# Kernel tuning notes

Hardware: AMD Instinct MI355X
Metric: run time of the kernel (lower is better)

The kernel has to match this reference:

```python
import jax, jax.numpy as jnp
import numpy as np

B = 16384      # number of ragged groups (batch)
SEG = 50       # history length per group -> sum(size)
TGT = 10       # targets per group -> sum(target_size)
H = 64         # hidden_size
NU = 1_000_000 # num_users
NI = 1_000_000 # num_items
TOTAL = B * SEG
T = B * TGT


def setup_inputs() -> dict:
    key = jax.random.key(0)
    k1, k2, k3, k4, k5 = jax.random.split(key, 5)
    user = jax.random.randint(k1, (TOTAL,), 0, NU)
    item = jax.random.randint(k2, (TOTAL,), 0, NI)
    target_item = jax.random.randint(k3, (T,), 0, NI)
    size = jnp.full((B,), SEG, dtype=jnp.int32)
    target_size = jnp.full((B,), TGT, dtype=jnp.int32)
    # nn.init.normal_(w, 0.0, 1e-4)
    user_weight = jax.random.normal(k4, (NU, H), dtype=jnp.float32) * 1e-4
    item_weight = jax.random.normal(k5, (NI, H), dtype=jnp.float32) * 1e-4
    return {"user": user, "item": item, "target_item": target_item,
            "size": size, "target_size": target_size,
            "user_weight": user_weight, "item_weight": item_weight}


def _center_l2(x):
    # F.normalize(x - x.mean(-1, keepdims=True), dim=-1)
    x = x - x.mean(axis=-1, keepdims=True)
    n = jnp.sqrt(jnp.sum(x * x, axis=-1, keepdims=True))
    return x / jnp.maximum(n, 1e-12)


def reference(user, item, target_item, size, target_size, user_weight, item_weight):
    nb = size.shape[0]
    total = item.shape[0]
    t = target_item.shape[0]
    # last user index of each segment: cumsum(size) - 1
    last_idx = jnp.cumsum(size) - 1
    user_emb = user_weight[user[last_idx]]                      # [B, H]
    item_emb = item_weight[item]                                # [total, H]
    seg_ids = jnp.repeat(jnp.arange(nb), size, total_repeat_length=total)
    seg_sum = jax.ops.segment_sum(item_emb, seg_ids, num_segments=nb)  # [B, H]
    item_mean = seg_sum / (size.astype(seg_sum.dtype)[:, None] + 1e-6)
    emb = 0.5 * user_emb + 0.5 * item_mean                      # [B, H]
    emb = jnp.repeat(emb, target_size, axis=0, total_repeat_length=t)  # [T, H]
    tgt_emb = item_weight[target_item]                          # [T, H]
    emb = _center_l2(emb)
    tgt_emb = _center_l2(tgt_emb)
    simplex = jnp.sum(emb * tgt_emb, axis=-1)                   # [T]
    return simplex
```

## Files before the change

### kernel.cpp

```cpp
#include <hip/hip_runtime.h>

#define HDIM 64

__device__ __forceinline__ float sub16_sum(float v) {
  v += __shfl_xor(v, 1);
  v += __shfl_xor(v, 2);
  v += __shfl_xor(v, 4);
  v += __shfl_xor(v, 8);
  return v;
}

__global__ void scan_offsets(const int* __restrict__ size,
                             const int* __restrict__ tsize, int B,
                             int* __restrict__ seg_off,
                             int* __restrict__ tgt_off) {
  __shared__ int s1[256];
  __shared__ int s2[256];
  const int t = threadIdx.x;
  const int per = (B + 255) >> 8;
  const int base = t * per;
  int sum1 = 0, sum2 = 0;
  for (int i = 0; i < per; ++i) {
    const int j = base + i;
    if (j < B) { sum1 += size[j]; sum2 += tsize[j]; }
  }
  s1[t] = sum1; s2[t] = sum2;
  __syncthreads();
  for (int d = 1; d < 256; d <<= 1) {
    const int a1 = (t >= d) ? s1[t - d] : 0;
    const int a2 = (t >= d) ? s2[t - d] : 0;
    __syncthreads();
    s1[t] += a1; s2[t] += a2;
    __syncthreads();
  }
  int ex1 = (t > 0) ? s1[t - 1] : 0;
  int ex2 = (t > 0) ? s2[t - 1] : 0;
  for (int i = 0; i < per; ++i) {
    const int j = base + i;
    if (j < B) {
      seg_off[j] = ex1; tgt_off[j] = ex2;
      ex1 += size[j];   ex2 += tsize[j];
    }
  }
}

__global__ __launch_bounds__(256) void simplex_kernel(
    const int* __restrict__ user, const int* __restrict__ item,
    const int* __restrict__ target_item, const int* __restrict__ size,
    const int* __restrict__ tsize, const float* __restrict__ uw,
    const float* __restrict__ iw, const int* __restrict__ seg_off,
    const int* __restrict__ tgt_off, float* __restrict__ out, int B,
    int useg, int utgt) {
  const int g = (int)((blockIdx.x * blockDim.x + threadIdx.x) >> 6);
  if (g >= B) return;
  const int lane = threadIdx.x & 63;
  const int sub = lane >> 4;
  const int c4 = lane & 15;

  const int sz = size[g];
  const int tn = tsize[g];
  int off, toff;
  if (seg_off) { off = seg_off[g]; toff = tgt_off[g]; }
  else         { off = g * useg;   toff = g * utgt; }

  float4 acc = make_float4(0.f, 0.f, 0.f, 0.f);
  for (int base = 0; base < sz; base += 64) {
    const int nrem = sz - base;
    const int nchunk = nrem < 64 ? nrem : 64;
    const int idx = (lane < nrem) ? item[off + base + lane] : 0;
#pragma unroll
    for (int i = 0; i < 64; i += 4) {
      const int r = i + sub;
      const int row = __shfl(idx, r);
      if (r < nchunk) {
        const float4 v = *reinterpret_cast<const float4*>(
            iw + (size_t)row * HDIM + (c4 << 2));
        acc.x += v.x; acc.y += v.y; acc.z += v.z; acc.w += v.w;
      }
    }
  }
  acc.x += __shfl_xor(acc.x, 16); acc.y += __shfl_xor(acc.y, 16);
  acc.z += __shfl_xor(acc.z, 16); acc.w += __shfl_xor(acc.w, 16);
  acc.x += __shfl_xor(acc.x, 32); acc.y += __shfl_xor(acc.y, 32);
  acc.z += __shfl_xor(acc.z, 32); acc.w += __shfl_xor(acc.w, 32);

  const float inv_sz = 1.0f / ((float)sz + 1e-6f);

  const int u = user[off + sz - 1];
  const float4 ue = *reinterpret_cast<const float4*>(
      uw + (size_t)u * HDIM + (c4 << 2));

  float4 e;
  e.x = 0.5f * ue.x + 0.5f * (acc.x * inv_sz);
  e.y = 0.5f * ue.y + 0.5f * (acc.y * inv_sz);
  e.z = 0.5f * ue.z + 0.5f * (acc.z * inv_sz);
  e.w = 0.5f * ue.w + 0.5f * (acc.w * inv_sz);

  const float mu = sub16_sum(e.x + e.y + e.z + e.w) * (1.0f / 64.0f);
  e.x -= mu; e.y -= mu; e.z -= mu; e.w -= mu;
  const float ss = sub16_sum(e.x * e.x + e.y * e.y + e.z * e.z + e.w * e.w);
  const float einv = 1.0f / fmaxf(sqrtf(ss), 1e-12f);
  e.x *= einv; e.y *= einv; e.z *= einv; e.w *= einv;

  for (int tb = 0; tb < tn; tb += 64) {
    const int trem = tn - tb;
    const int tch = trem < 64 ? trem : 64;
    const int tidx = (lane < trem) ? target_item[toff + tb + lane] : 0;
    for (int j = 0; j < tch; j += 4) {
      const int r = j + sub;
      const bool valid = r < tch;
      const int row = __shfl(tidx, r);
      float4 tv = make_float4(0.f, 0.f, 0.f, 0.f);
      if (valid) {
        tv = *reinterpret_cast<const float4*>(
            iw + (size_t)row * HDIM + (c4 << 2));
      }
      const float tmu = sub16_sum(tv.x + tv.y + tv.z + tv.w) * (1.0f / 64.0f);
      tv.x -= tmu; tv.y -= tmu; tv.z -= tmu; tv.w -= tmu;
      float tss = tv.x * tv.x + tv.y * tv.y + tv.z * tv.z + tv.w * tv.w;
      float dt  = e.x * tv.x + e.y * tv.y + e.z * tv.z + e.w * tv.w;
#pragma unroll
      for (int m = 1; m <= 8; m <<= 1) {
        tss += __shfl_xor(tss, m);
        dt  += __shfl_xor(dt, m);
      }
      if (valid && c4 == 0) {
        out[toff + tb + r] = dt / fmaxf(sqrtf(tss), 1e-12f);
      }
    }
  }
}

extern "C" void kernel_launch(void* const* d_in, const int* in_sizes, int n_in,
                              void* d_out, int out_size, void* d_ws,
                              size_t ws_size, hipStream_t stream) {
  const int* user        = (const int*)d_in[0];
  const int* item        = (const int*)d_in[1];
  const int* target_item = (const int*)d_in[2];
  const int* size        = (const int*)d_in[3];
  const int* tsize       = (const int*)d_in[4];
  const float* uw        = (const float*)d_in[5];
  const float* iw        = (const float*)d_in[6];
  float* out             = (float*)d_out;

  const int TOTAL = in_sizes[0];
  const int T     = in_sizes[2];
  const int B     = in_sizes[3];
  const int useg  = TOTAL / B;
  const int utgt  = T / B;

  int* seg_off = nullptr;
  int* tgt_off = nullptr;
  if (ws_size >= (size_t)2 * (size_t)B * sizeof(int)) {
    seg_off = (int*)d_ws;
    tgt_off = seg_off + B;
    scan_offsets<<<1, 256, 0, stream>>>(size, tsize, B, seg_off, tgt_off);
  }

  const int block = 256;
  const long long threads = (long long)B * 64;
  const int grid = (int)((threads + block - 1) / block);
  simplex_kernel<<<grid, block, 0, stream>>>(user, item, target_item, size,
                                             tsize, uw, iw, seg_off, tgt_off,
                                             out, B, useg, utgt);
}
```

Measured before the change: 500.5 us.

## Parallelize offset scan and batch all gathers upfront in fast path

Replaces the single-block offset scan with a two-level multi-block scan (per-block scan plus a one-wave scan of block totals), removing a serial prologue kernel. Adds a fast path for segments of at most 64 items and 16 targets that issues all 16 history-row loads, 4 target-row loads and the user-row load before any arithmetic, so many gathers are in flight at once. Branches in the loops are replaced by clamped indices and zero-weight FMAs. This raises register pressure and adds one extra kernel launch, and out-of-range rows are fetched redundantly.

```diff
diff --git a/kernel.cpp b/kernel.cpp
--- a/kernel.cpp
+++ b/kernel.cpp
@@ -1,6 +1,54 @@
 #include <hip/hip_runtime.h>
 
 #define HDIM 64
+
+
+__global__ __launch_bounds__(256) void scan_blocks(
+    const int* __restrict__ size, const int* __restrict__ tsize, int B,
+    int* __restrict__ seg_loc, int* __restrict__ tgt_loc,
+    int* __restrict__ seg_tot, int* __restrict__ tgt_tot) {
+  __shared__ int s1[256];
+  __shared__ int s2[256];
+  const int t = threadIdx.x;
+  const int i = blockIdx.x * 256 + t;
+  const int a = (i < B) ? size[i] : 0;
+  const int b = (i < B) ? tsize[i] : 0;
+  s1[t] = a; s2[t] = b;
+  __syncthreads();
+#pragma unroll
+  for (int d = 1; d < 256; d <<= 1) {
+    const int v1 = (t >= d) ? s1[t - d] : 0;
+    const int v2 = (t >= d) ? s2[t - d] : 0;
+    __syncthreads();
+    s1[t] += v1; s2[t] += v2;
+    __syncthreads();
+  }
+  if (i < B) { seg_loc[i] = s1[t] - a; tgt_loc[i] = s2[t] - b; }
+  if (t == 255) { seg_tot[blockIdx.x] = s1[255]; tgt_tot[blockIdx.x] = s2[255]; }
+}
+
+__global__ void scan_totals(int nb, int* __restrict__ seg_tot,
+                            int* __restrict__ tgt_tot,
+                            int* __restrict__ seg_base,
+                            int* __restrict__ tgt_base) {
+  const int lane = threadIdx.x & 63;
+  int c1 = 0, c2 = 0;
+  for (int base = 0; base < nb; base += 64) {
+    const int i = base + lane;
+    const int a0 = (i < nb) ? seg_tot[i] : 0;
+    const int b0 = (i < nb) ? tgt_tot[i] : 0;
+    int a = a0, b = b0;
+#pragma unroll
+    for (int d = 1; d < 64; d <<= 1) {
+      const int xa = __shfl_up(a, d);
+      const int xb = __shfl_up(b, d);
+      if (lane >= d) { a += xa; b += xb; }
+    }
+    if (i < nb) { seg_base[i] = c1 + a - a0; tgt_base[i] = c2 + b - b0; }
+    c1 += __shfl(a, 63);
+    c2 += __shfl(b, 63);
+  }
+}
 
 __device__ __forceinline__ float sub16_sum(float v) {
   v += __shfl_xor(v, 1);
@@ -10,46 +58,13 @@
   return v;
 }
 
-__global__ void scan_offsets(const int* __restrict__ size,
-                             const int* __restrict__ tsize, int B,
-                             int* __restrict__ seg_off,
-                             int* __restrict__ tgt_off) {
-  __shared__ int s1[256];
-  __shared__ int s2[256];
-  const int t = threadIdx.x;
-  const int per = (B + 255) >> 8;
-  const int base = t * per;
-  int sum1 = 0, sum2 = 0;
-  for (int i = 0; i < per; ++i) {
-    const int j = base + i;
-    if (j < B) { sum1 += size[j]; sum2 += tsize[j]; }
-  }
-  s1[t] = sum1; s2[t] = sum2;
-  __syncthreads();
-  for (int d = 1; d < 256; d <<= 1) {
-    const int a1 = (t >= d) ? s1[t - d] : 0;
-    const int a2 = (t >= d) ? s2[t - d] : 0;
-    __syncthreads();
-    s1[t] += a1; s2[t] += a2;
-    __syncthreads();
-  }
-  int ex1 = (t > 0) ? s1[t - 1] : 0;
-  int ex2 = (t > 0) ? s2[t - 1] : 0;
-  for (int i = 0; i < per; ++i) {
-    const int j = base + i;
-    if (j < B) {
-      seg_off[j] = ex1; tgt_off[j] = ex2;
-      ex1 += size[j];   ex2 += tsize[j];
-    }
-  }
-}
-
 __global__ __launch_bounds__(256) void simplex_kernel(
     const int* __restrict__ user, const int* __restrict__ item,
     const int* __restrict__ target_item, const int* __restrict__ size,
     const int* __restrict__ tsize, const float* __restrict__ uw,
-    const float* __restrict__ iw, const int* __restrict__ seg_off,
-    const int* __restrict__ tgt_off, float* __restrict__ out, int B,
+    const float* __restrict__ iw, const int* __restrict__ seg_loc,
+    const int* __restrict__ tgt_loc, const int* __restrict__ seg_base,
+    const int* __restrict__ tgt_base, float* __restrict__ out, int B,
     int useg, int utgt) {
   const int g = (int)((blockIdx.x * blockDim.x + threadIdx.x) >> 6);
   if (g >= B) return;
@@ -60,10 +75,84 @@
   const int sz = size[g];
   const int tn = tsize[g];
   int off, toff;
-  if (seg_off) { off = seg_off[g]; toff = tgt_off[g]; }
-  else         { off = g * useg;   toff = g * utgt; }
+  if (seg_loc) {
+    off = seg_base[g >> 8] + seg_loc[g];
+    toff = tgt_base[g >> 8] + tgt_loc[g];
+  } else {
+    off = g * useg;
+    toff = g * utgt;
+  }
+
+  const int szc = (sz > 0) ? sz : 1;
+  const int tnc = (tn > 0) ? tn : 1;
 
   float4 acc = make_float4(0.f, 0.f, 0.f, 0.f);
+
+  if (sz <= 64 && tn <= 16) {
+    const int idx = item[off + ((lane < szc) ? lane : (szc - 1))];
+    const int tidx = target_item[toff + ((lane < tnc) ? lane : (tnc - 1))];
+    const int u = user[off + szc - 1];
+
+    float4 sv[16];
+#pragma unroll
+    for (int p = 0; p < 16; ++p) {
+      const int r = p * 4 + sub;
+      const int row = __shfl(idx, (r < szc) ? r : (szc - 1));
+      sv[p] = *reinterpret_cast<const float4*>(iw + ((size_t)row << 6) + (c4 << 2));
+    }
+    float4 tv[4];
+#pragma unroll
+    for (int p = 0; p < 4; ++p) {
+      const int r = p * 4 + sub;
+      const int row = __shfl(tidx, (r < tnc) ? r : (tnc - 1));
+      tv[p] = *reinterpret_cast<const float4*>(iw + ((size_t)row << 6) + (c4 << 2));
+    }
+    const float4 ue = *reinterpret_cast<const float4*>(uw + ((size_t)u << 6) + (c4 << 2));
+
+#pragma unroll
+    for (int p = 0; p < 16; ++p) {
+      const int r = p * 4 + sub;
+      const float w = (r < sz) ? 1.0f : 0.0f;
+      acc.x = fmaf(sv[p].x, w, acc.x);
+      acc.y = fmaf(sv[p].y, w, acc.y);
+      acc.z = fmaf(sv[p].z, w, acc.z);
+      acc.w = fmaf(sv[p].w, w, acc.w);
+    }
+    acc.x += __shfl_xor(acc.x, 16); acc.y += __shfl_xor(acc.y, 16);
+    acc.z += __shfl_xor(acc.z, 16); acc.w += __shfl_xor(acc.w, 16);
+    acc.x += __shfl_xor(acc.x, 32); acc.y += __shfl_xor(acc.y, 32);
+    acc.z += __shfl_xor(acc.z, 32); acc.w += __shfl_xor(acc.w, 32);
+
+    const float inv_sz = 1.0f / ((float)sz + 1e-6f);
+    float4 e;
+    e.x = 0.5f * ue.x + 0.5f * (acc.x * inv_sz);
+    e.y = 0.5f * ue.y + 0.5f * (acc.y * inv_sz);
+    e.z = 0.5f * ue.z + 0.5f * (acc.z * inv_sz);
+    e.w = 0.5f * ue.w + 0.5f * (acc.w * inv_sz);
+
+    const float mu = sub16_sum(e.x + e.y + e.z + e.w) * (1.0f / 64.0f);
+    e.x -= mu; e.y -= mu; e.z -= mu; e.w -= mu;
+    const float ss = sub16_sum(e.x * e.x + e.y * e.y + e.z * e.z + e.w * e.w);
+    const float einv = 1.0f / fmaxf(sqrtf(ss), 1e-12f);
+    e.x *= einv; e.y *= einv; e.z *= einv; e.w *= einv;
+
+#pragma unroll
+    for (int p = 0; p < 4; ++p) {
+      const int r = p * 4 + sub;
+      float4 t = tv[p];
+      const float tmu = sub16_sum(t.x + t.y + t.z + t.w) * (1.0f / 64.0f);
+      t.x -= tmu; t.y -= tmu; t.z -= tmu; t.w -= tmu;
+      float tss = t.x * t.x + t.y * t.y + t.z * t.z + t.w * t.w;
+      float dt  = e.x * t.x + e.y * t.y + e.z * t.z + e.w * t.w;
+      tss = sub16_sum(tss);
+      dt  = sub16_sum(dt);
+      if (r < tn && c4 == 0) {
+        out[toff + r] = dt / fmaxf(sqrtf(tss), 1e-12f);
+      }
+    }
+    return;
+  }
+
   for (int base = 0; base < sz; base += 64) {
     const int nrem = sz - base;
     const int nchunk = nrem < 64 ? nrem : 64;
@@ -71,12 +160,13 @@
 #pragma unroll
     for (int i = 0; i < 64; i += 4) {
       const int r = i + sub;
-      const int row = __shfl(idx, r);
-      if (r < nchunk) {
-        const float4 v = *reinterpret_cast<const float4*>(
-            iw + (size_t)row * HDIM + (c4 << 2));
-        acc.x += v.x; acc.y += v.y; acc.z += v.z; acc.w += v.w;
-      }
+      const int row = __shfl(idx, (r < nchunk) ? r : 0);
+      const float w = (r < nchunk) ? 1.0f : 0.0f;
+      const float4 v = *reinterpret_cast<const float4*>(iw + ((size_t)row << 6) + (c4 << 2));
+      acc.x = fmaf(v.x, w, acc.x);
+      acc.y = fmaf(v.y, w, acc.y);
+      acc.z = fmaf(v.z, w, acc.z);
+      acc.w = fmaf(v.w, w, acc.w);
     }
   }
   acc.x += __shfl_xor(acc.x, 16); acc.y += __shfl_xor(acc.y, 16);
@@ -85,10 +175,8 @@
   acc.z += __shfl_xor(acc.z, 32); acc.w += __shfl_xor(acc.w, 32);
 
   const float inv_sz = 1.0f / ((float)sz + 1e-6f);
-
-  const int u = user[off + sz - 1];
-  const float4 ue = *reinterpret_cast<const float4*>(
-      uw + (size_t)u * HDIM + (c4 << 2));
+  const int u = user[off + szc - 1];
+  const float4 ue = *reinterpret_cast<const float4*>(uw + ((size_t)u << 6) + (c4 << 2));
 
   float4 e;
   e.x = 0.5f * ue.x + 0.5f * (acc.x * inv_sz);
@@ -109,21 +197,14 @@
     for (int j = 0; j < tch; j += 4) {
       const int r = j + sub;
       const bool valid = r < tch;
-      const int row = __shfl(tidx, r);
-      float4 tv = make_float4(0.f, 0.f, 0.f, 0.f);
-      if (valid) {
-        tv = *reinterpret_cast<const float4*>(
-            iw + (size_t)row * HDIM + (c4 << 2));
-      }
-      const float tmu = sub16_sum(tv.x + tv.y + tv.z + tv.w) * (1.0f / 64.0f);
-      tv.x -= tmu; tv.y -= tmu; tv.z -= tmu; tv.w -= tmu;
-      float tss = tv.x * tv.x + tv.y * tv.y + tv.z * tv.z + tv.w * tv.w;
-      float dt  = e.x * tv.x + e.y * tv.y + e.z * tv.z + e.w * tv.w;
-#pragma unroll
-      for (int m = 1; m <= 8; m <<= 1) {
-        tss += __shfl_xor(tss, m);
-        dt  += __shfl_xor(dt, m);
-      }
+      const int row = __shfl(tidx, valid ? r : 0);
+      float4 t = *reinterpret_cast<const float4*>(iw + ((size_t)row << 6) + (c4 << 2));
+      const float tmu = sub16_sum(t.x + t.y + t.z + t.w) * (1.0f / 64.0f);
+      t.x -= tmu; t.y -= tmu; t.z -= tmu; t.w -= tmu;
+      float tss = t.x * t.x + t.y * t.y + t.z * t.z + t.w * t.w;
+      float dt  = e.x * t.x + e.y * t.y + e.z * t.z + e.w * t.w;
+      tss = sub16_sum(tss);
+      dt  = sub16_sum(dt);
       if (valid && c4 == 0) {
         out[toff + tb + r] = dt / fmaxf(sqrtf(tss), 1e-12f);
       }
@@ -146,21 +227,31 @@
   const int TOTAL = in_sizes[0];
   const int T     = in_sizes[2];
   const int B     = in_sizes[3];
-  const int useg  = TOTAL / B;
-  const int utgt  = T / B;
-
-  int* seg_off = nullptr;
-  int* tgt_off = nullptr;
-  if (ws_size >= (size_t)2 * (size_t)B * sizeof(int)) {
-    seg_off = (int*)d_ws;
-    tgt_off = seg_off + B;
-    scan_offsets<<<1, 256, 0, stream>>>(size, tsize, B, seg_off, tgt_off);
+  const int useg  = (B > 0) ? TOTAL / B : 0;
+  const int utgt  = (B > 0) ? T / B : 0;
+
+  const int nb = (B + 255) >> 8;
+  int* seg_loc = nullptr; int* tgt_loc = nullptr;
+  int* seg_tot = nullptr; int* tgt_tot = nullptr;
+  int* seg_base = nullptr; int* tgt_base = nullptr;
+  const size_t need = ((size_t)2 * B + (size_t)4 * nb) * sizeof(int);
+  if (ws_size >= need) {
+    seg_loc  = (int*)d_ws;
+    tgt_loc  = seg_loc + B;
+    seg_tot  = tgt_loc + B;
+    tgt_tot  = seg_tot + nb;
+    seg_base = tgt_tot + nb;
+    tgt_base = seg_base + nb;
+    scan_blocks<<<nb, 256, 0, stream>>>(size, tsize, B, seg_loc, tgt_loc,
+                                        seg_tot, tgt_tot);
+    scan_totals<<<1, 64, 0, stream>>>(nb, seg_tot, tgt_tot, seg_base, tgt_base);
   }
 
   const int block = 256;
   const long long threads = (long long)B * 64;
   const int grid = (int)((threads + block - 1) / block);
   simplex_kernel<<<grid, block, 0, stream>>>(user, item, target_item, size,
-                                             tsize, uw, iw, seg_off, tgt_off,
-                                             out, B, useg, utgt);
-}
+                                             tsize, uw, iw, seg_loc, tgt_loc,
+                                             seg_base, tgt_base, out, B, useg,
+                                             utgt);
+}
```

Result: faster. 439.9 us (-12.1%).
